# Kernel tuning notes

Hardware: AMD Instinct MI355X
Metric: run time of the kernel (lower is better)

The kernel has to match this reference:

```python
import jax, jax.numpy as jnp
import numpy as np

IN_DIM = 32000   # source vocab
OUT_DIM = 32000  # target vocab
HID = 1024
MAXLEN = 32      # decode steps
B = 64
SRC_LEN = 256


def _lstm_bias(h):
    # Keras LSTM: unit_forget_bias=True -> forget-gate bias = 1, rest 0. Gate order i,f,g,o.
    return jnp.concatenate([jnp.zeros(h), jnp.ones(h), jnp.zeros(2 * h)])


def setup_inputs() -> dict:
    key = jax.random.key(0)
    ks = jax.random.split(key, 12)
    g = lambda k, shape, s=0.02: (jax.random.normal(k, shape, jnp.float32) * s)
    return {
        "source": jax.random.randint(ks[0], (B, SRC_LEN), 0, IN_DIM, jnp.int32),
        "enc_emb": g(ks[1], (IN_DIM, HID)),
        "enc_K": g(ks[2], (HID, 4 * HID)),
        "enc_R": g(ks[3], (HID, 4 * HID)),
        "enc_b": _lstm_bias(HID),
        "dec_emb": g(ks[4], (OUT_DIM, HID)),
        "dec_K": g(ks[5], (HID, 4 * HID)),
        "dec_R": g(ks[6], (HID, 4 * HID)),
        "dec_b": _lstm_bias(HID),
        "W_a": g(ks[7], (HID, HID)),
        "W_c": g(ks[8], (2 * HID, HID)),
        "b_c": jnp.zeros(HID, jnp.float32),
        "W_out": g(ks[9], (HID, OUT_DIM)),
        "b_out": jnp.zeros(OUT_DIM, jnp.float32),
    }


def _lstm_cell(x, h, c, K, R, b):
    z = x @ K + h @ R + b
    i, f, g, o = jnp.split(z, 4, axis=-1)
    c = jax.nn.sigmoid(f) * c + jax.nn.sigmoid(i) * jnp.tanh(g)
    h = jax.nn.sigmoid(o) * jnp.tanh(c)
    return h, c


def reference(source, enc_emb, enc_K, enc_R, enc_b,
              dec_emb, dec_K, dec_R, dec_b,
              W_a, W_c, b_c, W_out, b_out):
    bsz = source.shape[0]
    hid = enc_K.shape[0]

    # ----- Encoder (mask_zero=True: skip state update where source==0) -----
    xe = enc_emb[source]                      # [B,T,H]
    mask = source > 0                         # [B,T]

    def enc_step(carry, xm):
        h, c = carry
        x, m = xm                             # x [B,H], m [B]
        hn, cn = _lstm_cell(x, h, c, enc_K, enc_R, enc_b)
        m = m[:, None]
        return (jnp.where(m, hn, h), jnp.where(m, cn, c)), jnp.where(m, hn, h)

    h0 = jnp.zeros((bsz, hid), xe.dtype)
    (he, ce), hs_t = jax.lax.scan(enc_step, (h0, h0),
                                  (xe.transpose(1, 0, 2), mask.T))
    hs = hs_t.transpose(1, 0, 2)              # [B,T,H] encoder states

    # ----- Decoder loop (greedy argmax feedback) -----
    hsW = hs @ W_a                            # [B,T,H], precomputed attention keys
    amask = mask[:, None, :].astype(hs.dtype)  # [B,1,T]

    def dec_step(carry, _):
        y, h, c = carry                       # y [B] int32
        x = dec_emb[y]                        # [B,H]
        hn, cn = _lstm_cell(x, h, c, dec_K, dec_R, dec_b)
        ht = hn[:, None, :]                   # [B,1,H]
        # Luong attention with source mask (exp -> mask -> normalize, as in source)
        sc = jnp.einsum('bqh,bkh->bqk', ht, hsW)        # [B,1,T]
        sc = jnp.exp(sc - sc.max(-1, keepdims=True)) * amask
        a = sc / sc.sum(-1, keepdims=True)
        ctx = jnp.einsum('bqk,bkh->bqh', a, hs)          # [B,1,H]
        ah = jnp.tanh(jnp.concatenate([ctx, ht], -1) @ W_c + b_c)
        prob = jax.nn.softmax(ah @ W_out + b_out, axis=-1)[:, 0, :]  # [B,V]
        yn = jnp.argmax(prob, axis=-1).astype(jnp.int32)
        return (yn, hn, cn), prob

    y0 = jnp.ones((bsz,), jnp.int32)          # start token = 1 (tf.ones)
    _, outs = jax.lax.scan(dec_step, (y0, he, ce), None, length=MAXLEN)
    return outs.transpose(1, 0, 2)            # [B, MAXLEN, OUT_DIM]
```

## Files before the change

### kernel.cpp

```cpp
#include <hip/hip_runtime.h>
#include <hip/hip_bf16.h>

typedef __hip_bfloat16 bf16;
typedef short bf8v __attribute__((ext_vector_type(8)));
typedef float f32x4 __attribute__((ext_vector_type(4)));

#define DEVINL __device__ __forceinline__
#define MFMA16(a, b, c) __builtin_amdgcn_mfma_f32_16x16x32_bf16((a), (b), (c), 0, 0, 0)

DEVINL float us2f(unsigned short u) { unsigned v = ((unsigned)u) << 16; return __uint_as_float(v); }
DEVINL float b2f(bf16 x) { return __bfloat162float(x); }
DEVINL bf16 f2b(float x) { return __float2bfloat16(x); }
DEVINL float sigf(float x) { return 1.0f / (1.0f + expf(-x)); }
DEVINL unsigned short f2bu(float f) { bf16 h = __float2bfloat16(f); return *(unsigned short*)&h; }

DEVINL void gload16(const void* g, void* l) {
  __builtin_amdgcn_global_load_lds((const __attribute__((address_space(1))) void*)g,
                                   (__attribute__((address_space(3))) void*)l, 16, 0, 0);
}

DEVINL unsigned ald(const unsigned* p) {
  return __hip_atomic_load(p, __ATOMIC_RELAXED, __HIP_MEMORY_SCOPE_AGENT);
}
DEVINL void ast(unsigned* p, unsigned v) {
// ... 9 lines not shown
    unsigned g = blockIdx.x >> 5;
    unsigned* grp = bars + (g * 2 + s) * 16;
    unsigned* top = bars + (16 + s) * 16;
    unsigned* gen = bars + 288;
    unsigned t = __hip_atomic_fetch_add(grp, 1u, __ATOMIC_RELAXED, __HIP_MEMORY_SCOPE_AGENT);
    if (t == 31u) {
      ast(grp, 0u);
      unsigned tt = __hip_atomic_fetch_add(top, 1u, __ATOMIC_RELAXED, __HIP_MEMORY_SCOPE_AGENT);
      if (tt == 7u) {
        ast(top, 0u);
        asm volatile("s_waitcnt vmcnt(0)");
        ast(gen, lgen + 1u);
      }
    }
    while (ald(gen) <= lgen) __builtin_amdgcn_s_sleep(4);
  }
  __syncthreads();
}

#define OKPT_H  ((size_t)0)
#define OKPT_L  ((size_t)8388608)
#define ORPT_H  ((size_t)16777216)
#define ORPT_L  ((size_t)25165824)
#define OWAT    ((size_t)33554432)
#define OXE_H   ((size_t)35651584)
#define OXE_L   ((size_t)69206016)
#define OHSF5   ((size_t)35651584)
#define OHSB5   ((size_t)102760448)
#define XCH     ((size_t)136314880)
#define OHPK_E0 (XCH + 0)
// ... 8 lines not shown
#define OBARS5  (XCH + 1901568)
#define OXK_L5  ((size_t)138412032)
#define OWCT_H  ((size_t)0)
#define OWCT_L  ((size_t)4194304)
#define OPCTX5  ((size_t)8388608)
#define OWOT5   ((size_t)138412032)
#define OKRTH5  ((size_t)203948032)
#define OKRTL5  ((size_t)220725248)
#define OHSW5   ((size_t)237502464)

#define DELTA   1e-4f

#define D_LH   0
#define D_LL   32768
#define D_ZS   65536
#define D_AST  0
#define D_E    0
#define D_HBF  0
#define D_PSC  4096
#define D_EK   8448
#define D_PC4  8704
#define D_ZS3  0
#define D_PSC2 33024
#define D_GMX  37376
#define D_CCN  41536
#define D_CAND 41600
#define D_YL   131072
#define D_INV  131136
#define D_RT   131200

__global__ void ed_zero_v5(float4* p, int n) {
  int i = blockIdx.x * 256 + threadIdx.x;
  if (i < n) p[i] = make_float4(0.f, 0.f, 0.f, 0.f);
}

__global__ void ed_transpose_v5(const float* __restrict__ in, bf16* __restrict__ out,
                                int R, int C, int ostride, int ooff, int perm) {
  __shared__ float tile[32][33];
  int c0 = blockIdx.x * 32, r0 = blockIdx.y * 32;
  int tx = threadIdx.x & 31, ty0 = threadIdx.x >> 5;
#pragma unroll
  for (int i = 0; i < 4; i++) {
    int ty = ty0 + i * 8;
    tile[ty][tx] = in[(size_t)(r0 + ty) * C + c0 + tx];
  }
  __syncthreads();
#pragma unroll
  for (int i = 0; i < 4; i++) {
    int ty = ty0 + i * 8;
    int c = c0 + ty;
    int oc = perm ? ((c & 1023) * 4 + (c >> 10)) : c;
    out[(size_t)oc * ostride + ooff + r0 + tx] = f2b(tile[tx][ty]);
  }
}

__global__ void ed_transpose_split_v5(const float* __restrict__ in, bf16* __restrict__ oh,
                                      bf16* __restrict__ ol, int R, int C, int ostride,
                                      int ooff, int perm) {
  __shared__ float tile[32][33];
  int c0 = blockIdx.x * 32, r0 = blockIdx.y * 32;
  int tx = threadIdx.x & 31, ty0 = threadIdx.x >> 5;
#pragma unroll
  for (int i = 0; i < 4; i++) {
    int ty = ty0 + i * 8;
    tile[ty][tx] = in[(size_t)(r0 + ty) * C + c0 + tx];
  }
  __syncthreads();
#pragma unroll
  for (int i = 0; i < 4; i++) {
    int ty = ty0 + i * 8;
    int c = c0 + ty;
    int oc = perm ? ((c & 1023) * 4 + (c >> 10)) : c;
    float v = tile[tx][ty];
    bf16 hh = f2b(v);
    size_t o = (size_t)oc * ostride + ooff + r0 + tx;
    oh[o] = hh;
    ol[o] = f2b(v - b2f(hh));
  }
}

__global__ void ed_gather_split_v5(const int* __restrict__ src, const float* __restrict__ emb,
                                   bf16* __restrict__ xh, bf16* __restrict__ xl) {
  int bid = blockIdx.x;
  int t = bid >> 6, b = bid & 63;
  int tok = src[b * 256 + t];
  const float* rowp = emb + (size_t)tok * 1024;
  int i = threadIdx.x * 4;
  float4 v = *(const float4*)(rowp + i);
  bf16 h0 = f2b(v.x), h1 = f2b(v.y), h2 = f2b(v.z), h3 = f2b(v.w);
  ushort4 oh, ol;
  oh.x = *(unsigned short*)&h0; oh.y = *(unsigned short*)&h1;
  oh.z = *(unsigned short*)&h2; oh.w = *(unsigned short*)&h3;
  ol.x = f2bu(v.x - b2f(h0)); ol.y = f2bu(v.y - b2f(h1));
  ol.z = f2bu(v.z - b2f(h2)); ol.w = f2bu(v.w - b2f(h3));
  *(ushort4*)(xh + (size_t)bid * 1024 + i) = oh;
  *(ushort4*)(xl + (size_t)bid * 1024 + i) = ol;
}

__global__ __launch_bounds__(256, 2) void ed_gemm_bt_v5(
    const bf16* __restrict__ A, const bf16* __restrict__ BT, bf16* __restrict__ C,
    int M, int N, int K) {
  __shared__ __align__(16) bf16 As[128 * 32];
  __shared__ __align__(16) bf16 Bs[128 * 32];
  int m0 = blockIdx.y * 128, n0 = blockIdx.x * 128;
  int tid = threadIdx.x, w = tid >> 6, l = tid & 63;
  int wm = w >> 1, wn = w & 1;
  int lr = l & 15, lq = l >> 4;
  f32x4 acc[4][4] = {};
  for (int k0 = 0; k0 < K; k0 += 32) {
    __syncthreads();
#pragma unroll
    for (int j = 0; j < 2; j++) {
      int o = (w * 2 + j) * 1024 + l * 16;
      int rrow = o >> 6, kk = (o & 63) >> 1;
// ... 9 lines not shown
        bf8v b = *(const bf8v*)(Bs + (wn * 64 + ni * 16 + lr) * 32 + lq * 8);
        acc[mi][ni] = MFMA16(a, b, acc[mi][ni]);
      }
    }
  }
#pragma unroll
  for (int mi = 0; mi < 4; mi++)
#pragma unroll
    for (int ni = 0; ni < 4; ni++)
#pragma unroll
      for (int r = 0; r < 4; r++)
        C[(size_t)(m0 + wm * 64 + mi * 16 + lq * 4 + r) * N + n0 + wn * 64 + ni * 16 + lr] =
            f2b(acc[mi][ni][r]);
}

__global__ __launch_bounds__(256, 2) void ed_gemm3_v5(
    const bf16* __restrict__ Ah, const bf16* __restrict__ Al,
    const bf16* __restrict__ Bh, const bf16* __restrict__ Bl,
    bf16* __restrict__ Ch, bf16* __restrict__ Cl, int M, int N, int K) {
  __shared__ __align__(16) bf16 Ash[128 * 32];
  __shared__ __align__(16) bf16 Asl[128 * 32];
  __shared__ __align__(16) bf16 Bsh[128 * 32];
  __shared__ __align__(16) bf16 Bsl[128 * 32];
  int m0 = blockIdx.y * 128, n0 = blockIdx.x * 128;
  int tid = threadIdx.x, w = tid >> 6, l = tid & 63;
  int wm = w >> 1, wn = w & 1;
  int lr = l & 15, lq = l >> 4;
  f32x4 acc[4][4] = {};
  for (int k0 = 0; k0 < K; k0 += 32) {
    __syncthreads();
#pragma unroll
// ... 22 lines not shown
  }
#pragma unroll
  for (int mi = 0; mi < 4; mi++)
#pragma unroll
    for (int ni = 0; ni < 4; ni++)
#pragma unroll
      for (int r = 0; r < 4; r++) {
        float v = acc[mi][ni][r];
        bf16 hh = f2b(v);
        size_t idx = (size_t)(m0 + wm * 64 + mi * 16 + lq * 4 + r) * N + n0 + wn * 64 + ni * 16 + lr;
        Ch[idx] = hh;
        Cl[idx] = f2b(v - b2f(hh));
      }
}

__global__ __launch_bounds__(1024, 4) void ed_enc_v5(
    const int* __restrict__ src, const bf16* __restrict__ Rh, const bf16* __restrict__ Rl,
    const bf16* __restrict__ Xh, const bf16* __restrict__ Xl, const float* __restrict__ enc_b,
    unsigned* hpk0, unsigned* hpk1, float* __restrict__ cbuf,
    float* __restrict__ hsf, bf16* __restrict__ hsb, unsigned* bars) {
  extern __shared__ char sm[];
  bf16* lh = (bf16*)sm;
  bf16* ll = (bf16*)(sm + 32768);
  float* zs = (float*)(sm + 65536);
  float* xkf = (float*)(sm + 82944);
  int bid = blockIdx.x, tid = threadIdx.x;
  int bg = bid >> 6, cg = bid & 63;
  int wv = tid >> 6, l = tid & 63, lr = l & 15, lq = l >> 4;
  int kq = wv >> 2, cs = wv & 3;
  int srow = tid >> 6, sj0 = (tid & 63) * 16;
  int grow = tid >> 4, gul = tid & 15;
  bf8v Rh_[8], Rl_[8];
  {
    const bf16* bh = Rh + (size_t)(cg * 64 + cs * 16 + lr) * 1024 + kq * 256 + lq * 8;
    const bf16* bl = Rl + (size_t)(cg * 64 + cs * 16 + lr) * 1024 + kq * 256 + lq * 8;
#pragma unroll
    for (int i = 0; i < 8; i++) {
      Rh_[i] = *(const bf8v*)(bh + i * 32);
      Rl_[i] = *(const bf8v*)(bl + i * 32);
    }
  }
  float bi[4];
// ... 12 lines not shown
      const unsigned* hrow = hc + (size_t)(bg * 16 + srow) * 1024 + sj0;
      unsigned u[16];
#pragma unroll
      for (int j = 0; j < 16; j++) u[j] = ald(hrow + j);
      int r8 = (srow & 7) << 3;
#pragma unroll
      for (int j = 0; j < 16; j += 2) {
        int es = (sj0 + j) ^ r8;
        *(unsigned*)((char*)lh + srow * 2048 + es * 2) = (u[j] >> 16) | (u[j + 1] & 0xffff0000u);
        *(unsigned*)((char*)ll + srow * 2048 + es * 2) = (u[j] & 0xffffu) | (u[j + 1] << 16);
      }
    }
    {
      int xr = tid >> 6, xc = tid & 63;
      size_t xi = ((size_t)t * 64 + bg * 16 + xr) * 4096 + cg * 64 + xc;
      xkf[xr * 64 + xc] = us2f(*(const unsigned short*)(Xh + xi)) +
                          us2f(*(const unsigned short*)(Xl + xi));
    }
    __syncthreads();
    {
      f32x4 acc = {0.f, 0.f, 0.f, 0.f};
      int r8 = (lr & 7) << 3;
#pragma unroll
      for (int i = 0; i < 8; i++) {
        int e0 = kq * 256 + i * 32 + lq * 8;
        int es = e0 ^ r8;
        bf8v a_h = *(const bf8v*)((char*)lh + lr * 2048 + es * 2);
        bf8v a_l = *(const bf8v*)((char*)ll + lr * 2048 + es * 2);
        acc = MFMA16(a_h, Rh_[i], acc);
        acc = MFMA16(a_h, Rl_[i], acc);
        acc = MFMA16(a_l, Rh_[i], acc);
        acc = MFMA16(a_l, Rl_[i], acc);
// ... 12 lines not shown
                zs[(32 + grow) * 68 + cc] + zs[(48 + grow) * 68 + cc] +
                xkf[grow * 64 + cc] + bi[g];
      }
      float iv = sigf(zz[0]), fv = sigf(zz[1]), gv = tanhf(zz[2]), ov = sigf(zz[3]);
      float cn = fv * c_ + iv * gv;
      float hnv = ov * tanhf(cn);
      bool m = src[b_ * 256 + t] > 0;
      int es = u ^ ((grow & 7) << 3);
      float hold = b2f(*(const bf16*)((char*)lh + grow * 2048 + es * 2)) +
                   b2f(*(const bf16*)((char*)ll + grow * 2048 + es * 2));
      float hv = m ? hnv : hold;
      c_ = m ? cn : c_;
      unsigned short uh = f2bu(hv);
      unsigned pkv = ((unsigned)uh << 16) | (unsigned)f2bu(hv - us2f(uh));
      ast(hn + (size_t)b_ * 1024 + u, pkv);
      hsf[((size_t)t * 64 + b_) * 1024 + u] = hv;
      hsb[((size_t)t * 64 + b_) * 1024 + u] = f2b(hv);
    }
    gridbar2(bars, lgen);
    lgen++;
    unsigned* tp = hc; hc = hn; hn = tp;
  }
  if (tid < 256) cbuf[(size_t)(bg * 16 + grow) * 1024 + cg * 16 + gul] = c_;
}

DEVINL void dec_lstm5(int bg, int cgl, int tid, char* sm,
                      const unsigned* hc, unsigned* hn,
                      const float* __restrict__ dec_emb,
                      const bf16* __restrict__ Kh, const bf16* __restrict__ Kl,
                      const float* __restrict__ dec_b, float& c_) {
  {
    int srow = tid >> 6, sj0 = (tid & 63) * 16;
    const unsigned* hrow = hc + (size_t)(bg * 16 + srow) * 1024 + sj0;
    unsigned u[16];
#pragma unroll
    for (int j = 0; j < 16; j++) u[j] = ald(hrow + j);
    int r8 = (srow & 7) << 3;
    bf16* lh = (bf16*)(sm + D_LH);
    bf16* ll = (bf16*)(sm + D_LL);
#pragma unroll
    for (int j = 0; j < 16; j += 2) {
      int es = (sj0 + j) ^ r8;
      *(unsigned*)((char*)lh + srow * 2048 + es * 2) = (u[j] >> 16) | (u[j + 1] & 0xffff0000u);
      *(unsigned*)((char*)ll + srow * 2048 + es * 2) = (u[j] & 0xffffu) | (u[j + 1] << 16);
    }
  }
  __syncthreads();
  int wv = tid >> 6, l = tid & 63, lr = l & 15, lq = l >> 4;
  int kq = wv >> 2, cs = wv & 3;
  const int* y_l = (const int*)(sm + D_YL);
  float* zs = (float*)(sm + D_ZS);
  {
    f32x4 acc = {0.f, 0.f, 0.f, 0.f};
    const bf16* bh = Kh + (size_t)(cgl * 64 + cs * 16 + lr) * 2048;
    const bf16* bl = Kl + (size_t)(cgl * 64 + cs * 16 + lr) * 2048;
    if (kq < 2) {
      const float* xr = dec_emb + (size_t)y_l[lr] * 1024 + kq * 512 + lq * 8;
#pragma unroll 4
      for (int i = 0; i < 16; i++) {
        float4 v0 = *(const float4*)(xr + i * 32);
        float4 v1 = *(const float4*)(xr + i * 32 + 4);
        float vs[8] = {v0.x, v0.y, v0.z, v0.w, v1.x, v1.y, v1.z, v1.w};
        bf8v a_h, a_l;
#pragma unroll
        for (int e = 0; e < 8; e++) {
          unsigned short uh = f2bu(vs[e]);
          a_h[e] = (short)uh;
          a_l[e] = (short)f2bu(vs[e] - us2f(uh));
        }
        int k = kq * 512 + i * 32 + lq * 8;
        bf8v b_h = *(const bf8v*)(bh + k);
        bf8v b_l = *(const bf8v*)(bl + k);
        acc = MFMA16(a_h, b_h, acc); acc = MFMA16(a_h, b_l, acc);
        acc = MFMA16(a_l, b_h, acc); acc = MFMA16(a_l, b_l, acc);
      }
    } else {
      bf16* lh = (bf16*)(sm + D_LH);
      bf16* ll = (bf16*)(sm + D_LL);
      int r8 = (lr & 7) << 3;
#pragma unroll 4
      for (int i = 0; i < 16; i++) {
        int k2 = (kq - 2) * 512 + i * 32 + lq * 8;
        int es = k2 ^ r8;
        bf8v a_h = *(const bf8v*)((char*)lh + lr * 2048 + es * 2);
        bf8v a_l = *(const bf8v*)((char*)ll + lr * 2048 + es * 2);
        int k = 1024 + k2;
        bf8v b_h = *(const bf8v*)(bh + k);
        bf8v b_l = *(const bf8v*)(bl + k);
        acc = MFMA16(a_h, b_h, acc); acc = MFMA16(a_h, b_l, acc);
        acc = MFMA16(a_l, b_h, acc); acc = MFMA16(a_l, b_l, acc);
      }
    }
#pragma unroll
    for (int r = 0; r < 4; r++) zs[(kq * 16 + lq * 4 + r) * 68 + cs * 16 + lr] = acc[r];
  }
  __syncthreads();
  if (tid < 256) {
    int grow = tid >> 4, gul = tid & 15;
    int b_ = bg * 16 + grow;
    float zz[4];
#pragma unroll
    for (int g = 0; g < 4; g++) {
      int cc = gul * 4 + g;
      int colp = cgl * 64 + cc;
      float v = zs[(0 + grow) * 68 + cc] + zs[(16 + grow) * 68 + cc] +
                zs[(32 + grow) * 68 + cc] + zs[(48 + grow) * 68 + cc];
      zz[g] = v + dec_b[(colp & 3) * 1024 + (colp >> 2)];
    }
    float iv = sigf(zz[0]), fv = sigf(zz[1]), gv = tanhf(zz[2]), ov = sigf(zz[3]);
    float cn = fv * c_ + iv * gv;
    c_ = cn;
    float hv = ov * tanhf(cn);
    unsigned short uh = f2bu(hv);
    unsigned pkv = ((unsigned)uh << 16) | (unsigned)f2bu(hv - us2f(uh));
    ast(hn + (size_t)b_ * 1024 + cgl * 16 + gul, pkv);
  }
}

__global__ __launch_bounds__(1024, 4) void ed_dec_v5(
    const int* __restrict__ src,
    const bf16* __restrict__ KRh, const bf16* __restrict__ KRl, const float* __restrict__ dec_b,
    const bf16* __restrict__ WcTh, const bf16* __restrict__ WcTl, const float* __restrict__ b_cp,
    const bf16* __restrict__ WoTh, const float* __restrict__ b_op,
    const float* __restrict__ Wout_f32, const float* __restrict__ dec_emb,
    const float* __restrict__ hsf, const bf16* __restrict__ hsW,
    unsigned* hpkA, unsigned* hpkB, float* __restrict__ cbuf,
    float* __restrict__ pctx, float* __restrict__ psum, unsigned* ahpk,
    float* __restrict__ rowsum, float* __restrict__ rmax, int* __restrict__ ridx,
    float* __restrict__ out, unsigned* bars) {
  extern __shared__ char sm[];
  int bid = blockIdx.x, tid = threadIdx.x;
  int bg = bid >> 6, cgl = bid & 63;
  int wv = tid >> 6, l = tid & 63, lr = l & 15, lq = l >> 4;
  float c_ = 0.f;
  if (tid < 256) c_ = cbuf[(size_t)(bg * 16 + (tid >> 4)) * 1024 + cgl * 16 + (tid & 15)];
  unsigned *hc = hpkA, *hn = hpkB;
  unsigned lgen = 0;

  if (tid < 16) ((int*)(sm + D_YL))[tid] = 1;
  __syncthreads();
  dec_lstm5(bg, cgl, tid, sm, hc, hn, dec_emb, KRh, KRl, dec_b, c_);
  gridbar2(bars, lgen); lgen++;
  { unsigned* tp = hc; hc = hn; hn = tp; }

  for (int st = 0; st < 32; st++) {
    {
      int b_ = bid >> 2, kg = bid & 3;
      float* hbf = (float*)(sm + D_HBF);
      hbf[tid] = us2f((unsigned short)(ald(hc + (size_t)b_ * 1024 + tid) >> 16));
      __syncthreads();
      float* psc = (float*)(sm + D_PSC);
      {
        int kl = tid >> 4, q = tid & 15;
        const bf16* wrow = hsW + ((size_t)(kg * 64 + kl) * 64 + b_) * 1024 + q * 64;
        float p = 0.f;
#pragma unroll
        for (int j = 0; j < 8; j++) {
// ... 31 lines not shown
        pc4[kc * 1024 + cq * 4 + 2] = a2;
        pc4[kc * 1024 + cq * 4 + 3] = a3;
      }
      __syncthreads();
      {
        float v = pc4[tid] + pc4[1024 + tid] + pc4[2048 + tid] + pc4[3072 + tid];
        astf(pctx + ((size_t)kg * 64 + b_) * 1024 + tid, v);
      }
      if (tid == 0) {
        float* ek2 = (float*)(sm + D_EK);
        float s_ = 0.f;
        for (int i2 = 0; i2 < 64; i2++) s_ += ek2[i2];
        astf(psum + kg * 64 + b_, s_);
      }
    }
    gridbar2(bars, lgen); lgen++;
    {
      float* inv_l = (float*)(sm + D_INV);
      if (tid < 16) {
        int rb = bg * 16 + tid;
        float sg = aldf(psum + rb) + aldf(psum + 64 + rb) +
                   aldf(psum + 128 + rb) + aldf(psum + 192 + rb);
        inv_l[tid] = 1.0f / sg;
      }
      __syncthreads();
      float* zs3 = (float*)(sm + D_ZS3);
      {
        int kq = wv;
        f32x4 acc = {0.f, 0.f, 0.f, 0.f};
        const bf16* bh = WcTh + (size_t)(cgl * 16 + lr) * 2048;
        const bf16* bl = WcTl + (size_t)(cgl * 16 + lr) * 2048;
// ... 30 lines not shown
        for (int r = 0; r < 4; r++) zs3[(kq * 16 + lq * 4 + r) * 17 + lr] = acc[r];
      }
      __syncthreads();
      if (tid < 256) {
        int grow = tid >> 4, gcol = tid & 15;
        float v = 0.f;
#pragma unroll
        for (int q = 0; q < 16; q++) v += zs3[(q * 16 + grow) * 17 + gcol];
        v += b_cp[cgl * 16 + gcol];
        float ahv = tanhf(v);
        unsigned short uh = f2bu(ahv);
        unsigned pkv = ((unsigned)uh << 16) | (unsigned)f2bu(ahv - us2f(uh));
        ast(ahpk + (size_t)(bg * 16 + grow) * 1024 + cgl * 16 + gcol, pkv);
      }
    }
    gridbar2(bars, lgen); lgen++;
    {
      int base = bid * 125;
      bf16* Ast = (bf16*)(sm + D_AST);
      {
        int row = tid >> 4, k0 = (tid & 15) * 64;
        const unsigned* ap = ahpk + (size_t)row * 1024 + k0;
        int r8 = (row & 7) << 3;
#pragma unroll
        for (int j = 0; j < 64; j += 2) {
          unsigned u0 = ald(ap + j), u1 = ald(ap + j + 1);
          int es = (k0 + j) ^ r8;
          *(unsigned*)((char*)Ast + row * 2048 + es * 2) = (u0 >> 16) | (u1 & 0xffff0000u);
        }
      }
      __syncthreads();
      int rg = wv >> 2, cg2 = wv & 3;
      f32x4 la0 = {0.f, 0.f, 0.f, 0.f}, la1 = {0.f, 0.f, 0.f, 0.f};
      {
        int c0 = cg2 * 32 + lr;      int cc0 = c0 < 125 ? c0 : 124;
        int c1 = cg2 * 32 + 16 + lr; int cc1 = c1 < 125 ? c1 : 124;
        const bf16* w0 = WoTh + (size_t)(base + cc0) * 1024;
        const bf16* w1 = WoTh + (size_t)(base + cc1) * 1024;
        int r8 = ((rg * 16 + lr) & 7) << 3;
#pragma unroll 4
        for (int i = 0; i < 32; i++) {
          int k = i * 32 + lq * 8;
          int es = k ^ r8;
          bf8v a_h = *(const bf8v*)((char*)Ast + (rg * 16 + lr) * 2048 + es * 2);
          la0 = MFMA16(a_h, *(const bf8v*)(w0 + k), la0);
          la1 = MFMA16(a_h, *(const bf8v*)(w1 + k), la1);
        }
      }
      __syncthreads();
      float* e = (float*)(sm + D_E);
      {
#pragma unroll
        for (int ct = 0; ct < 2; ct++) {
          int cl = cg2 * 32 + ct * 16 + lr;
          if (cl < 125) {
#pragma unroll
            for (int r = 0; r < 4; r++) {
              float lv = (ct == 0 ? la0[r] : la1[r]) + b_op[base + cl];
              e[(rg * 16 + lq * 4 + r) * 129 + cl] = lv;
            }
          }
        }
      }
      __syncthreads();
      if (tid < 64) {
        float sm_ = 0.f, v1 = -1e30f, v2 = -1e30f;
        int i1 = 0, i2 = 0;
        for (int c2 = 0; c2 < 125; c2++) {
          float v = e[tid * 129 + c2];
          sm_ += expf(v);
          if (v > v1) { v2 = v1; i2 = i1; v1 = v; i1 = base + c2; }
          else if (v > v2) { v2 = v; i2 = base + c2; }
        }
        astf(rowsum + bid * 64 + tid, sm_);
        astf(rmax + (bid * 64 + tid) * 2 + 0, v1);
        ast((unsigned*)ridx + (bid * 64 + tid) * 2 + 0, (unsigned)i1);
        astf(rmax + (bid * 64 + tid) * 2 + 1, v2);
        ast((unsigned*)ridx + (bid * 64 + tid) * 2 + 1, (unsigned)i2);
      }
    }
    gridbar2(bars, lgen); lgen++;
    {
      float* psc2 = (float*)(sm + D_PSC2);
      {
        int rr = tid & 63, pp = tid >> 6;
        float s_ = 0.f;
#pragma unroll 4
        for (int cu = pp * 16; cu < pp * 16 + 16; cu++) s_ += aldf(rowsum + cu * 64 + rr);
        psc2[rr * 17 + pp] = s_;
      }
      __syncthreads();
      float* rt = (float*)(sm + D_RT);
      if (tid < 64) {
        float s_ = 0.f;
#pragma unroll
        for (int p2 = 0; p2 < 16; p2++) s_ += psc2[tid * 17 + p2];
        rt[tid] = s_;
      }
      __syncthreads();
      float* e = (float*)(sm + D_E);
      {
        int base = bid * 125;
        for (int i = tid; i < 8000; i += 1024) {
          int r_ = i / 125, c2 = i - r_ * 125;
          out[((size_t)r_ * 32 + st) * 32000 + base + c2] = expf(e[r_ * 129 + c2]) / rt[r_];
        }
      }
      if (st < 31) {
        float* gmx = (float*)(sm + D_GMX);
        int* ccnt = (int*)(sm + D_CCN);
        int* cand = (int*)(sm + D_CAND);
        int* y_l = (int*)(sm + D_YL);
        int r16 = tid & 15, ch = tid >> 4;
        int rowg = bg * 16 + r16;
        float vloc[8]; int iloc[8];
        {
          float m_ = -1e30f;
#pragma unroll
          for (int ee = 0; ee < 8; ee++) {
            int ent = ch * 8 + ee;
// ... 22 lines not shown
            }
          }
        }
        __syncthreads();
        {
          int row2 = wv;
          int rowg2 = bg * 16 + row2;
          int cnt = ccnt[row2]; if (cnt > 8) cnt = 8;
          double bv = -1e30; int bi_ = 0x7fffffff;
          for (int ci = 0; ci < cnt; ci++) {
            int c = cand[row2 * 8 + ci];
            double s_ = 0.0;
            for (int k = l; k < 1024; k += 64) {
              unsigned u = ald(ahpk + (size_t)rowg2 * 1024 + k);
              float av = us2f((unsigned short)(u >> 16)) + us2f((unsigned short)(u & 0xffffu));
              s_ += (double)av * (double)Wout_f32[(size_t)k * 32000 + c];
            }
#pragma unroll
            for (int off = 32; off > 0; off >>= 1) s_ += __shfl_down(s_, off);
            if (l == 0) {
              s_ += (double)b_op[c];
              if (s_ > bv || (s_ == bv && c < bi_)) { bv = s_; bi_ = c; }
            }
          }
          if (l == 0) y_l[row2] = bi_;
        }
        __syncthreads();
        dec_lstm5(bg, cgl, tid, sm, hc, hn, dec_emb, KRh, KRl, dec_b, c_);
      }
    }
    gridbar2(bars, lgen); lgen++;
    { unsigned* tp = hc; hc = hn; hn = tp; }
  }
}

extern "C" void kernel_launch(void* const* d_in, const int* in_sizes, int n_in,
                              void* d_out, int out_size, void* d_ws, size_t ws_size,
                              hipStream_t stream) {
  (void)in_sizes; (void)n_in; (void)out_size; (void)ws_size;
  const int*   src     = (const int*)  d_in[0];
  const float* enc_emb = (const float*)d_in[1];
  const float* enc_K   = (const float*)d_in[2];
  const float* enc_R   = (const float*)d_in[3];
  const float* enc_b   = (const float*)d_in[4];
  const float* dec_emb = (const float*)d_in[5];
  const float* dec_K   = (const float*)d_in[6];
  const float* dec_R   = (const float*)d_in[7];
  const float* dec_b   = (const float*)d_in[8];
  const float* W_a     = (const float*)d_in[9];
  const float* W_c     = (const float*)d_in[10];
  const float* b_c     = (const float*)d_in[11];
  const float* W_out   = (const float*)d_in[12];
  const float* b_out   = (const float*)d_in[13];
  char* ws = (char*)d_ws;

  hipFuncSetAttribute((const void*)ed_enc_v5, hipFuncAttributeMaxDynamicSharedMemorySize, 163840);
  hipFuncSetAttribute((const void*)ed_dec_v5, hipFuncAttributeMaxDynamicSharedMemorySize, 163840);

  bf16* KpTh = (bf16*)(ws + OKPT_H);
  bf16* KpTl = (bf16*)(ws + OKPT_L);
  bf16* RpTh = (bf16*)(ws + ORPT_H);
  bf16* RpTl = (bf16*)(ws + ORPT_L);
  bf16* WaT  = (bf16*)(ws + OWAT);
  bf16* xeh  = (bf16*)(ws + OXE_H);
  bf16* xel  = (bf16*)(ws + OXE_L);
  float* hsf = (float*)(ws + OHSF5);
  bf16* hsb  = (bf16*)(ws + OHSB5);
  unsigned* hpkE0 = (unsigned*)(ws + OHPK_E0);
  unsigned* hpkE1 = (unsigned*)(ws + OHPK_E1);
  unsigned* hpkD0 = (unsigned*)(ws + OHPK_D0);
  float* cbuf = (float*)(ws + OCBUF5);
  unsigned* ahpk = (unsigned*)(ws + OAHPK);
  float* rsum = (float*)(ws + ORSUM5);
  float* rmaxp = (float*)(ws + ORMAX5);
  int*  ridxp = (int*)(ws + ORIDX5);
  float* psum = (float*)(ws + OPSUM5);
  unsigned* bars = (unsigned*)(ws + OBARS5);
  bf16* XkL  = (bf16*)(ws + OXK_L5);
  bf16* XkH  = (bf16*)d_out;
  bf16* WcTh = (bf16*)(ws + OWCT_H);
  bf16* WcTl = (bf16*)(ws + OWCT_L);
  float* pctx = (float*)(ws + OPCTX5);
  bf16* WoTh = (bf16*)(ws + OWOT5);
  bf16* KRTh = (bf16*)(ws + OKRTH5);
  bf16* KRTl = (bf16*)(ws + OKRTL5);
  bf16* hsW  = (bf16*)(ws + OHSW5);

  ed_zero_v5<<<512, 256, 0, stream>>>((float4*)(ws + XCH), 131072);
  ed_transpose_split_v5<<<dim3(128, 32), 256, 0, stream>>>(enc_K, KpTh, KpTl, 1024, 4096, 1024, 0, 1);
  ed_transpose_split_v5<<<dim3(128, 32), 256, 0, stream>>>(enc_R, RpTh, RpTl, 1024, 4096, 1024, 0, 1);
  ed_transpose_v5<<<dim3(32, 32), 256, 0, stream>>>(W_a, WaT, 1024, 1024, 1024, 0, 0);
  ed_gather_split_v5<<<16384, 256, 0, stream>>>(src, enc_emb, xeh, xel);
  ed_gemm3_v5<<<dim3(32, 128), 256, 0, stream>>>(xeh, xel, KpTh, KpTl, XkH, XkL, 16384, 4096, 1024);
  ed_transpose_split_v5<<<dim3(32, 64), 256, 0, stream>>>(W_c, WcTh, WcTl, 2048, 1024, 2048, 0, 0);
  ed_enc_v5<<<256, 1024, 87040, stream>>>(src, RpTh, RpTl, XkH, XkL, enc_b,
                                          hpkE0, hpkE1, cbuf, hsf, hsb, bars);
  ed_transpose_v5<<<dim3(1000, 32), 256, 0, stream>>>(W_out, WoTh, 1024, 32000, 1024, 0, 0);
  ed_transpose_split_v5<<<dim3(128, 32), 256, 0, stream>>>(dec_K, KRTh, KRTl, 1024, 4096, 2048, 0, 1);
  ed_transpose_split_v5<<<dim3(128, 32), 256, 0, stream>>>(dec_R, KRTh, KRTl, 1024, 4096, 2048, 1024, 1);
  ed_gemm_bt_v5<<<dim3(8, 128), 256, 0, stream>>>(hsb, WaT, hsW, 16384, 1024, 1024);
  ed_dec_v5<<<256, 1024, 131456, stream>>>(src, KRTh, KRTl, dec_b, WcTh, WcTl, b_c,
                                           WoTh, b_out, W_out, dec_emb, hsf, hsW,
                                           hpkE0, hpkD0, cbuf, pctx, psum, ahpk,
                                           rsum, rmaxp, ridxp, (float*)d_out, bars + 512);
}
```

Measured before the change: 15.11 ms.

## Use per-batch-group 64-block barriers and stage LSTM/logit weights through LDS

```diff
diff --git a/kernel.cpp b/kernel.cpp
--- a/kernel.cpp
+++ b/kernel.cpp
@@ -47,6 +47,28 @@
       }
     }
     while (ald(gen) <= lgen) __builtin_amdgcn_s_sleep(4);
+  }
+  __syncthreads();
+}
+
+DEVINL void bar64(unsigned* b, unsigned lgen, int lid) {
+  __syncthreads();
+  if (threadIdx.x == 0) {
+    unsigned s = lgen & 1;
+    unsigned* grp = b + (((unsigned)(lid >> 5) & 1u) * 2 + s) * 16;
+    unsigned* top = b + (4 + s) * 16;
+    unsigned* gen = b + 96;
+    unsigned t = __hip_atomic_fetch_add(grp, 1u, __ATOMIC_RELAXED, __HIP_MEMORY_SCOPE_AGENT);
+    if (t == 31u) {
+      ast(grp, 0u);
+      unsigned tt = __hip_atomic_fetch_add(top, 1u, __ATOMIC_RELAXED, __HIP_MEMORY_SCOPE_AGENT);
+      if (tt == 1u) {
+        ast(top, 0u);
+        asm volatile("s_waitcnt vmcnt(0)");
+        ast(gen, lgen + 1u);
+      }
+    }
+    while (ald(gen) <= lgen) __builtin_amdgcn_s_sleep(2);
   }
   __syncthreads();
 }
@@ -85,27 +107,30 @@
 #define D_LH   0
 #define D_LL   32768
 #define D_ZS   65536
-#define D_AST  0
-#define D_E    0
+#define D_KBH  83968
+#define D_KBL  116736
+#define D4_A   0
+#define D4_W   16384
+#define D4_E   49152
 #define D_HBF  0
 #define D_PSC  4096
 #define D_EK   8448
 #define D_PC4  8704
 #define D_ZS3  0
-#define D_PSC2 33024
-#define D_GMX  37376
-#define D_CCN  41536
-#define D_CAND 41600
-#define D_YL   131072
-#define D_INV  131136
-#define D_RT   131200
-
-__global__ void ed_zero_v5(float4* p, int n) {
+#define D_PSC2 0
+#define D_GMX  4352
+#define D_CCN  8512
+#define D_CAND 8576
+#define D_YL   149504
+#define D_INV  149568
+#define D_RT   149632
+
+__global__ void ed_zero_v6(float4* p, int n) {
   int i = blockIdx.x * 256 + threadIdx.x;
   if (i < n) p[i] = make_float4(0.f, 0.f, 0.f, 0.f);
 }
 
-__global__ void ed_transpose_v5(const float* __restrict__ in, bf16* __restrict__ out,
+__global__ void ed_transpose_v6(const float* __restrict__ in, bf16* __restrict__ out,
                                 int R, int C, int ostride, int ooff, int perm) {
   __shared__ float tile[32][33];
   int c0 = blockIdx.x * 32, r0 = blockIdx.y * 32;
@@ -125,7 +150,7 @@
   }
 }
 
-__global__ void ed_transpose_split_v5(const float* __restrict__ in, bf16* __restrict__ oh,
+__global__ void ed_transpose_split_v6(const float* __restrict__ in, bf16* __restrict__ oh,
                                       bf16* __restrict__ ol, int R, int C, int ostride,
                                       int ooff, int perm) {
   __shared__ float tile[32][33];
@@ -150,7 +175,7 @@
   }
 }
 
-__global__ void ed_gather_split_v5(const int* __restrict__ src, const float* __restrict__ emb,
+__global__ void ed_gather_split_v6(const int* __restrict__ src, const float* __restrict__ emb,
                                    bf16* __restrict__ xh, bf16* __restrict__ xl) {
   int bid = blockIdx.x;
   int t = bid >> 6, b = bid & 63;
@@ -168,7 +193,7 @@
   *(ushort4*)(xl + (size_t)bid * 1024 + i) = ol;
 }
 
-__global__ __launch_bounds__(256, 2) void ed_gemm_bt_v5(
+__global__ __launch_bounds__(256, 2) void ed_gemm_bt_v6(
     const bf16* __restrict__ A, const bf16* __restrict__ BT, bf16* __restrict__ C,
     int M, int N, int K) {
   __shared__ __align__(16) bf16 As[128 * 32];
@@ -208,7 +233,7 @@
             f2b(acc[mi][ni][r]);
 }
 
-__global__ __launch_bounds__(256, 2) void ed_gemm3_v5(
+__global__ __launch_bounds__(256, 2) void ed_gemm3_v6(
     const bf16* __restrict__ Ah, const bf16* __restrict__ Al,
     const bf16* __restrict__ Bh, const bf16* __restrict__ Bl,
     bf16* __restrict__ Ch, bf16* __restrict__ Cl, int M, int N, int K) {
@@ -261,18 +286,19 @@
       }
 }
 
-__global__ __launch_bounds__(1024, 4) void ed_enc_v5(
+__global__ __launch_bounds__(1024, 4) void ed_enc_v6(
     const int* __restrict__ src, const bf16* __restrict__ Rh, const bf16* __restrict__ Rl,
     const bf16* __restrict__ Xh, const bf16* __restrict__ Xl, const float* __restrict__ enc_b,
     unsigned* hpk0, unsigned* hpk1, float* __restrict__ cbuf,
-    float* __restrict__ hsf, bf16* __restrict__ hsb, unsigned* bars) {
+    float* __restrict__ hsf, bf16* __restrict__ hsb, unsigned* barsE) {
   extern __shared__ char sm[];
   bf16* lh = (bf16*)sm;
   bf16* ll = (bf16*)(sm + 32768);
   float* zs = (float*)(sm + 65536);
   float* xkf = (float*)(sm + 82944);
   int bid = blockIdx.x, tid = threadIdx.x;
-  int bg = bid >> 6, cg = bid & 63;
+  int bg = bid >> 6, cg = bid & 63, lid = bid & 63;
+  unsigned* barL = barsE + bg * 128;
   int wv = tid >> 6, l = tid & 63, lr = l & 15, lq = l >> 4;
   int kq = wv >> 2, cs = wv & 3;
   int srow = tid >> 6, sj0 = (tid & 63) * 16;
@@ -315,8 +341,9 @@
     {
       int xr = tid >> 6, xc = tid & 63;
       size_t xi = ((size_t)t * 64 + bg * 16 + xr) * 4096 + cg * 64 + xc;
-      xkf[xr * 64 + xc] = us2f(*(const unsigned short*)(Xh + xi)) +
-                          us2f(*(const unsigned short*)(Xl + xi));
+      unsigned short xh = __builtin_nontemporal_load((const unsigned short*)(Xh + xi));
+      unsigned short xl = __builtin_nontemporal_load((const unsigned short*)(Xl + xi));
+      xkf[xr * 64 + xc] = us2f(xh) + us2f(xl);
     }
     __syncthreads();
     {
@@ -359,86 +386,98 @@
       unsigned short uh = f2bu(hv);
       unsigned pkv = ((unsigned)uh << 16) | (unsigned)f2bu(hv - us2f(uh));
       ast(hn + (size_t)b_ * 1024 + u, pkv);
-      hsf[((size_t)t * 64 + b_) * 1024 + u] = hv;
-      hsb[((size_t)t * 64 + b_) * 1024 + u] = f2b(hv);
-    }
-    gridbar2(bars, lgen);
+      __builtin_nontemporal_store(hv, hsf + ((size_t)t * 64 + b_) * 1024 + u);
+      __builtin_nontemporal_store(f2bu(hv), (unsigned short*)(hsb + ((size_t)t * 64 + b_) * 1024 + u));
+    }
+    bar64(barL, lgen, lid);
     lgen++;
     unsigned* tp = hc; hc = hn; hn = tp;
   }
   if (tid < 256) cbuf[(size_t)(bg * 16 + grow) * 1024 + cg * 16 + gul] = c_;
 }
 
-DEVINL void dec_lstm5(int bg, int cgl, int tid, char* sm,
+DEVINL void dec_lstm6(int bg, int cgl, int tid, char* sm,
                       const unsigned* hc, unsigned* hn,
                       const float* __restrict__ dec_emb,
                       const bf16* __restrict__ Kh, const bf16* __restrict__ Kl,
                       const float* __restrict__ dec_b, float& c_) {
+  bf16* lh = (bf16*)(sm + D_LH);
+  bf16* ll = (bf16*)(sm + D_LL);
   {
-    int srow = tid >> 6, sj0 = (tid & 63) * 16;
-    const unsigned* hrow = hc + (size_t)(bg * 16 + srow) * 1024 + sj0;
+    int srow = tid >> 6, sl = tid & 63;
+    const unsigned* hrow = hc + (size_t)(bg * 16 + srow) * 1024 + sl * 16;
     unsigned u[16];
 #pragma unroll
     for (int j = 0; j < 16; j++) u[j] = ald(hrow + j);
-    int r8 = (srow & 7) << 3;
-    bf16* lh = (bf16*)(sm + D_LH);
-    bf16* ll = (bf16*)(sm + D_LL);
-#pragma unroll
-    for (int j = 0; j < 16; j += 2) {
-      int es = (sj0 + j) ^ r8;
-      *(unsigned*)((char*)lh + srow * 2048 + es * 2) = (u[j] >> 16) | (u[j + 1] & 0xffff0000u);
-      *(unsigned*)((char*)ll + srow * 2048 + es * 2) = (u[j] & 0xffffu) | (u[j + 1] << 16);
-    }
-  }
-  __syncthreads();
+    uint4 ha, hb, la, lb;
+    ha.x = (u[0] >> 16) | (u[1] & 0xffff0000u);  ha.y = (u[2] >> 16) | (u[3] & 0xffff0000u);
+    ha.z = (u[4] >> 16) | (u[5] & 0xffff0000u);  ha.w = (u[6] >> 16) | (u[7] & 0xffff0000u);
+    hb.x = (u[8] >> 16) | (u[9] & 0xffff0000u);  hb.y = (u[10] >> 16) | (u[11] & 0xffff0000u);
+    hb.z = (u[12] >> 16) | (u[13] & 0xffff0000u); hb.w = (u[14] >> 16) | (u[15] & 0xffff0000u);
+    la.x = (u[0] & 0xffffu) | (u[1] << 16);  la.y = (u[2] & 0xffffu) | (u[3] << 16);
+    la.z = (u[4] & 0xffffu) | (u[5] << 16);  la.w = (u[6] & 0xffffu) | (u[7] << 16);
+    lb.x = (u[8] & 0xffffu) | (u[9] << 16);  lb.y = (u[10] & 0xffffu) | (u[11] << 16);
+    lb.z = (u[12] & 0xffffu) | (u[13] << 16); lb.w = (u[14] & 0xffffu) | (u[15] << 16);
+    int swz = (srow & 7) << 4;
+    char* rbh = (char*)lh + srow * 2048;
+    char* rbl = (char*)ll + srow * 2048;
+    *(uint4*)(rbh + ((sl * 32) ^ swz)) = ha;
+    *(uint4*)(rbh + ((sl * 32 + 16) ^ swz)) = hb;
+    *(uint4*)(rbl + ((sl * 32) ^ swz)) = la;
+    *(uint4*)(rbl + ((sl * 32 + 16) ^ swz)) = lb;
+  }
   int wv = tid >> 6, l = tid & 63, lr = l & 15, lq = l >> 4;
-  int kq = wv >> 2, cs = wv & 3;
+  int kg2 = wv >> 2, cs = wv & 3;
+  bf16* kbh = (bf16*)(sm + D_KBH);
+  bf16* kbl = (bf16*)(sm + D_KBL);
   const int* y_l = (const int*)(sm + D_YL);
   float* zs = (float*)(sm + D_ZS);
-  {
-    f32x4 acc = {0.f, 0.f, 0.f, 0.f};
-    const bf16* bh = Kh + (size_t)(cgl * 64 + cs * 16 + lr) * 2048;
-    const bf16* bl = Kl + (size_t)(cgl * 64 + cs * 16 + lr) * 2048;
-    if (kq < 2) {
-      const float* xr = dec_emb + (size_t)y_l[lr] * 1024 + kq * 512 + lq * 8;
-#pragma unroll 4
-      for (int i = 0; i < 16; i++) {
-        float4 v0 = *(const float4*)(xr + i * 32);
-        float4 v1 = *(const float4*)(xr + i * 32 + 4);
+  f32x4 acc = {0.f, 0.f, 0.f, 0.f};
+  int colB = cs * 16 + lr;
+  int bswz = (colB & 7) << 4;
+  int aswz = (lr & 7) << 4;
+  for (int c = 0; c < 8; c++) {
+    __syncthreads();
+#pragma unroll
+    for (int r = 0; r < 2; r++) {
+      int i = wv * 128 + r * 64 + l;
+      int col = i >> 5, j = i & 31;
+      size_t se = (size_t)(cgl * 64 + col) * 2048 + c * 256 + ((size_t)(j ^ (col & 7)) << 3);
+      gload16(Kh + se, (char*)kbh + wv * 2048 + r * 1024);
+      gload16(Kl + se, (char*)kbl + wv * 2048 + r * 1024);
+    }
+    __syncthreads();
+#pragma unroll
+    for (int s = 0; s < 2; s++) {
+      int kl = kg2 * 64 + s * 32 + lq * 8;
+      bf8v b_h = *(const bf8v*)((char*)kbh + colB * 512 + ((kl * 2) ^ bswz));
+      bf8v b_l = *(const bf8v*)((char*)kbl + colB * 512 + ((kl * 2) ^ bswz));
+      int gk = c * 256 + kl;
+      bf8v a_h, a_l;
+      if (gk < 1024) {
+        const float* xr = dec_emb + (size_t)y_l[lr] * 1024 + gk;
+        float4 v0 = *(const float4*)xr;
+        float4 v1 = *(const float4*)(xr + 4);
         float vs[8] = {v0.x, v0.y, v0.z, v0.w, v1.x, v1.y, v1.z, v1.w};
-        bf8v a_h, a_l;
 #pragma unroll
         for (int e = 0; e < 8; e++) {
           unsigned short uh = f2bu(vs[e]);
           a_h[e] = (short)uh;
           a_l[e] = (short)f2bu(vs[e] - us2f(uh));
         }
-        int k = kq * 512 + i * 32 + lq * 8;
-        bf8v b_h = *(const bf8v*)(bh + k);
-        bf8v b_l = *(const bf8v*)(bl + k);
-        acc = MFMA16(a_h, b_h, acc); acc = MFMA16(a_h, b_l, acc);
-        acc = MFMA16(a_l, b_h, acc); acc = MFMA16(a_l, b_l, acc);
-      }
-    } else {
-      bf16* lh = (bf16*)(sm + D_LH);
-      bf16* ll = (bf16*)(sm + D_LL);
-      int r8 = (lr & 7) << 3;
-#pragma unroll 4
-      for (int i = 0; i < 16; i++) {
-        int k2 = (kq - 2) * 512 + i * 32 + lq * 8;
-        int es = k2 ^ r8;
-        bf8v a_h = *(const bf8v*)((char*)lh + lr * 2048 + es * 2);
-        bf8v a_l = *(const bf8v*)((char*)ll + lr * 2048 + es * 2);
-        int k = 1024 + k2;
-        bf8v b_h = *(const bf8v*)(bh + k);
-        bf8v b_l = *(const bf8v*)(bl + k);
-        acc = MFMA16(a_h, b_h, acc); acc = MFMA16(a_h, b_l, acc);
-        acc = MFMA16(a_l, b_h, acc); acc = MFMA16(a_l, b_l, acc);
-      }
-    }
-#pragma unroll
-    for (int r = 0; r < 4; r++) zs[(kq * 16 + lq * 4 + r) * 68 + cs * 16 + lr] = acc[r];
-  }
+      } else {
+        int hk = gk - 1024;
+        a_h = *(const bf8v*)((char*)lh + lr * 2048 + ((hk * 2) ^ aswz));
+        a_l = *(const bf8v*)((char*)ll + lr * 2048 + ((hk * 2) ^ aswz));
+      }
+      acc = MFMA16(a_h, b_h, acc);
+      acc = MFMA16(a_h, b_l, acc);
+      acc = MFMA16(a_l, b_h, acc);
+      acc = MFMA16(a_l, b_l, acc);
+    }
+  }
+#pragma unroll
+  for (int r = 0; r < 4; r++) zs[(kg2 * 16 + lq * 4 + r) * 68 + cs * 16 + lr] = acc[r];
   __syncthreads();
   if (tid < 256) {
     int grow = tid >> 4, gul = tid & 15;
@@ -462,7 +501,7 @@
   }
 }
 
-__global__ __launch_bounds__(1024, 4) void ed_dec_v5(
+__global__ __launch_bounds__(1024, 4) void ed_dec_v6(
     const int* __restrict__ src,
     const bf16* __restrict__ KRh, const bf16* __restrict__ KRl, const float* __restrict__ dec_b,
     const bf16* __restrict__ WcTh, const bf16* __restrict__ WcTl, const float* __restrict__ b_cp,
@@ -472,20 +511,21 @@
     unsigned* hpkA, unsigned* hpkB, float* __restrict__ cbuf,
     float* __restrict__ pctx, float* __restrict__ psum, unsigned* ahpk,
     float* __restrict__ rowsum, float* __restrict__ rmax, int* __restrict__ ridx,
-    float* __restrict__ out, unsigned* bars) {
+    float* __restrict__ out, unsigned* barsG, unsigned* barsL) {
   extern __shared__ char sm[];
   int bid = blockIdx.x, tid = threadIdx.x;
-  int bg = bid >> 6, cgl = bid & 63;
+  int bg = bid >> 6, cgl = bid & 63, lid = bid & 63;
+  unsigned* barL = barsL + bg * 128;
   int wv = tid >> 6, l = tid & 63, lr = l & 15, lq = l >> 4;
   float c_ = 0.f;
   if (tid < 256) c_ = cbuf[(size_t)(bg * 16 + (tid >> 4)) * 1024 + cgl * 16 + (tid & 15)];
   unsigned *hc = hpkA, *hn = hpkB;
-  unsigned lgen = 0;
+  unsigned lgenL = 0, lgenG = 0;
 
   if (tid < 16) ((int*)(sm + D_YL))[tid] = 1;
   __syncthreads();
-  dec_lstm5(bg, cgl, tid, sm, hc, hn, dec_emb, KRh, KRl, dec_b, c_);
-  gridbar2(bars, lgen); lgen++;
+  dec_lstm6(bg, cgl, tid, sm, hc, hn, dec_emb, KRh, KRl, dec_b, c_);
+  bar64(barL, lgenL, lid); lgenL++;
   { unsigned* tp = hc; hc = hn; hn = tp; }
 
   for (int st = 0; st < 32; st++) {
@@ -547,7 +587,7 @@
         astf(psum + kg * 64 + b_, s_);
       }
     }
-    gridbar2(bars, lgen); lgen++;
+    bar64(barL, lgenL, lid); lgenL++;
     {
       float* inv_l = (float*)(sm + D_INV);
       if (tid < 16) {
@@ -608,52 +648,63 @@
         ast(ahpk + (size_t)(bg * 16 + grow) * 1024 + cgl * 16 + gcol, pkv);
       }
     }
-    gridbar2(bars, lgen); lgen++;
+    gridbar2(barsG, lgenG); lgenG++;
     {
       int base = bid * 125;
-      bf16* Ast = (bf16*)(sm + D_AST);
+      bf16* abuf = (bf16*)(sm + D4_A);
+      bf16* wbuf = (bf16*)(sm + D4_W);
+      int rg = wv >> 2, cpair = wv & 3;
+      f32x4 acc0 = {0.f, 0.f, 0.f, 0.f}, acc1 = {0.f, 0.f, 0.f, 0.f};
+      for (int kc = 0; kc < 8; kc++) {
+        int k0 = kc * 128;
+        __syncthreads();
+        {
+          int row = tid >> 4, l16 = tid & 15;
+          const unsigned* ap = ahpk + (size_t)row * 1024 + k0 + l16 * 8;
+          unsigned u0 = ald(ap), u1 = ald(ap + 1), u2 = ald(ap + 2), u3 = ald(ap + 3);
+          unsigned u4 = ald(ap + 4), u5 = ald(ap + 5), u6 = ald(ap + 6), u7 = ald(ap + 7);
+          uint4 hv;
+          hv.x = (u0 >> 16) | (u1 & 0xffff0000u);
+          hv.y = (u2 >> 16) | (u3 & 0xffff0000u);
+          hv.z = (u4 >> 16) | (u5 & 0xffff0000u);
+          hv.w = (u6 >> 16) | (u7 & 0xffff0000u);
+          *(uint4*)((char*)abuf + row * 256 + ((l16 * 16) ^ ((row & 7) << 4))) = hv;
+        }
+#pragma unroll
+        for (int r = 0; r < 2; r++) {
+          int i = wv * 128 + r * 64 + l;
+          int col = i >> 4, j = i & 15;
+          int ccol = col < 125 ? col : 124;
+          size_t se = (size_t)(base + ccol) * 1024 + k0 + ((size_t)(j ^ (col & 7)) << 3);
+          gload16(WoTh + se, (char*)wbuf + wv * 2048 + r * 1024);
+        }
+        __syncthreads();
+#pragma unroll
+        for (int s = 0; s < 4; s++) {
+          int kl = s * 32 + lq * 8;
+          int ar = rg * 16 + lr;
+          bf8v a = *(const bf8v*)((char*)abuf + ar * 256 + ((kl * 2) ^ ((ar & 7) << 4)));
+          int c0 = cpair * 32 + lr, c1 = c0 + 16;
+          bf8v b0 = *(const bf8v*)((char*)wbuf + c0 * 256 + ((kl * 2) ^ ((c0 & 7) << 4)));
+          bf8v b1 = *(const bf8v*)((char*)wbuf + c1 * 256 + ((kl * 2) ^ ((c1 & 7) << 4)));
+          acc0 = MFMA16(a, b0, acc0);
+          acc1 = MFMA16(a, b1, acc1);
+        }
+      }
+      __syncthreads();
+      float* e = (float*)(sm + D4_E);
       {
-        int row = tid >> 4, k0 = (tid & 15) * 64;
-        const unsigned* ap = ahpk + (size_t)row * 1024 + k0;
-        int r8 = (row & 7) << 3;
-#pragma unroll
-        for (int j = 0; j < 64; j += 2) {
-          unsigned u0 = ald(ap + j), u1 = ald(ap + j + 1);
-          int es = (k0 + j) ^ r8;
-          *(unsigned*)((char*)Ast + row * 2048 + es * 2) = (u0 >> 16) | (u1 & 0xffff0000u);
-        }
-      }
-      __syncthreads();
-      int rg = wv >> 2, cg2 = wv & 3;
-      f32x4 la0 = {0.f, 0.f, 0.f, 0.f}, la1 = {0.f, 0.f, 0.f, 0.f};
-      {
-        int c0 = cg2 * 32 + lr;      int cc0 = c0 < 125 ? c0 : 124;
-        int c1 = cg2 * 32 + 16 + lr; int cc1 = c1 < 125 ? c1 : 124;
-        const bf16* w0 = WoTh + (size_t)(base + cc0) * 1024;
-        const bf16* w1 = WoTh + (size_t)(base + cc1) * 1024;
-        int r8 = ((rg * 16 + lr) & 7) << 3;
-#pragma unroll 4
-        for (int i = 0; i < 32; i++) {
-          int k = i * 32 + lq * 8;
-          int es = k ^ r8;
-          bf8v a_h = *(const bf8v*)((char*)Ast + (rg * 16 + lr) * 2048 + es * 2);
-          la0 = MFMA16(a_h, *(const bf8v*)(w0 + k), la0);
-          la1 = MFMA16(a_h, *(const bf8v*)(w1 + k), la1);
-        }
-      }
-      __syncthreads();
-      float* e = (float*)(sm + D_E);
-      {
-#pragma unroll
-        for (int ct = 0; ct < 2; ct++) {
-          int cl = cg2 * 32 + ct * 16 + lr;
-          if (cl < 125) {
-#pragma unroll
-            for (int r = 0; r < 4; r++) {
-              float lv = (ct == 0 ? la0[r] : la1[r]) + b_op[base + cl];
-              e[(rg * 16 + lq * 4 + r) * 129 + cl] = lv;
-            }
-          }
+        int cl0 = cpair * 32 + lr;
+        if (cl0 < 125) {
+#pragma unroll
+          for (int r = 0; r < 4; r++)
+            e[(rg * 16 + lq * 4 + r) * 129 + cl0] = acc0[r] + b_op[base + cl0];
+        }
+        int cl1 = cpair * 32 + 16 + lr;
+        if (cl1 < 125) {
+#pragma unroll
+          for (int r = 0; r < 4; r++)
+            e[(rg * 16 + lq * 4 + r) * 129 + cl1] = acc1[r] + b_op[base + cl1];
         }
       }
       __syncthreads();
@@ -673,7 +724,7 @@
         ast((unsigned*)ridx + (bid * 64 + tid) * 2 + 1, (unsigned)i2);
       }
     }
-    gridbar2(bars, lgen); lgen++;
+    gridbar2(barsG, lgenG); lgenG++;
     {
       float* psc2 = (float*)(sm + D_PSC2);
       {
@@ -692,12 +743,13 @@
         rt[tid] = s_;
       }
       __syncthreads();
-      float* e = (float*)(sm + D_E);
+      float* e = (float*)(sm + D4_E);
       {
         int base = bid * 125;
         for (int i = tid; i < 8000; i += 1024) {
           int r_ = i / 125, c2 = i - r_ * 125;
-          out[((size_t)r_ * 32 + st) * 32000 + base + c2] = expf(e[r_ * 129 + c2]) / rt[r_];
+          float pv = expf(e[r_ * 129 + c2]) / rt[r_];
+          __builtin_nontemporal_store(pv, out + ((size_t)r_ * 32 + st) * 32000 + base + c2);
         }
       }
       if (st < 31) {
@@ -750,7 +802,8 @@
             for (int k = l; k < 1024; k += 64) {
               unsigned u = ald(ahpk + (size_t)rowg2 * 1024 + k);
               float av = us2f((unsigned short)(u >> 16)) + us2f((unsigned short)(u & 0xffffu));
-              s_ += (double)av * (double)Wout_f32[(size_t)k * 32000 + c];
+              float wv_ = __builtin_nontemporal_load(Wout_f32 + (size_t)k * 32000 + c);
+              s_ += (double)av * (double)wv_;
             }
 #pragma unroll
             for (int off = 32; off > 0; off >>= 1) s_ += __shfl_down(s_, off);
@@ -762,10 +815,10 @@
           if (l == 0) y_l[row2] = bi_;
         }
         __syncthreads();
-        dec_lstm5(bg, cgl, tid, sm, hc, hn, dec_emb, KRh, KRl, dec_b, c_);
-      }
-    }
-    gridbar2(bars, lgen); lgen++;
+        dec_lstm6(bg, cgl, tid, sm, hc, hn, dec_emb, KRh, KRl, dec_b, c_);
+      }
+    }
+    bar64(barL, lgenL, lid); lgenL++;
     { unsigned* tp = hc; hc = hn; hn = tp; }
   }
 }
@@ -790,8 +843,8 @@
   const float* b_out   = (const float*)d_in[13];
   char* ws = (char*)d_ws;
 
-  hipFuncSetAttribute((const void*)ed_enc_v5, hipFuncAttributeMaxDynamicSharedMemorySize, 163840);
-  hipFuncSetAttribute((const void*)ed_dec_v5, hipFuncAttributeMaxDynamicSharedMemorySize, 163840);
+  hipFuncSetAttribute((const void*)ed_enc_v6, hipFuncAttributeMaxDynamicSharedMemorySize, 163840);
+  hipFuncSetAttribute((const void*)ed_dec_v6, hipFuncAttributeMaxDynamicSharedMemorySize, 163840);
 
   bf16* KpTh = (bf16*)(ws + OKPT_H);
   bf16* KpTl = (bf16*)(ws + OKPT_L);
@@ -811,7 +864,9 @@
   float* rmaxp = (float*)(ws + ORMAX5);
   int*  ridxp = (int*)(ws + ORIDX5);
   float* psum = (float*)(ws + OPSUM5);
-  unsigned* bars = (unsigned*)(ws + OBARS5);
+  unsigned* barsE = (unsigned*)(ws + OBARS5);
+  unsigned* barsG = (unsigned*)(ws + OBARS5 + 4096);
+  unsigned* barsL = (unsigned*)(ws + OBARS5 + 8192);
   bf16* XkL  = (bf16*)(ws + OXK_L5);
   bf16* XkH  = (bf16*)d_out;
   bf16* WcTh = (bf16*)(ws + OWCT_H);
@@ -822,21 +877,21 @@
   bf16* KRTl = (bf16*)(ws + OKRTL5);
   bf16* hsW  = (bf16*)(ws + OHSW5);
 
-  ed_zero_v5<<<512, 256, 0, stream>>>((float4*)(ws + XCH), 131072);
-  ed_transpose_split_v5<<<dim3(128, 32), 256, 0, stream>>>(enc_K, KpTh, KpTl, 1024, 4096, 1024, 0, 1);
-  ed_transpose_split_v5<<<dim3(128, 32), 256, 0, stream>>>(enc_R, RpTh, RpTl, 1024, 4096, 1024, 0, 1);
-  ed_transpose_v5<<<dim3(32, 32), 256, 0, stream>>>(W_a, WaT, 1024, 1024, 1024, 0, 0);
-  ed_gather_split_v5<<<16384, 256, 0, stream>>>(src, enc_emb, xeh, xel);
-  ed_gemm3_v5<<<dim3(32, 128), 256, 0, stream>>>(xeh, xel, KpTh, KpTl, XkH, XkL, 16384, 4096, 1024);
-  ed_transpose_split_v5<<<dim3(32, 64), 256, 0, stream>>>(W_c, WcTh, WcTl, 2048, 1024, 2048, 0, 0);
-  ed_enc_v5<<<256, 1024, 87040, stream>>>(src, RpTh, RpTl, XkH, XkL, enc_b,
-                                          hpkE0, hpkE1, cbuf, hsf, hsb, bars);
-  ed_transpose_v5<<<dim3(1000, 32), 256, 0, stream>>>(W_out, WoTh, 1024, 32000, 1024, 0, 0);
-  ed_transpose_split_v5<<<dim3(128, 32), 256, 0, stream>>>(dec_K, KRTh, KRTl, 1024, 4096, 2048, 0, 1);
-  ed_transpose_split_v5<<<dim3(128, 32), 256, 0, stream>>>(dec_R, KRTh, KRTl, 1024, 4096, 2048, 1024, 1);
-  ed_gemm_bt_v5<<<dim3(8, 128), 256, 0, stream>>>(hsb, WaT, hsW, 16384, 1024, 1024);
-  ed_dec_v5<<<256, 1024, 131456, stream>>>(src, KRTh, KRTl, dec_b, WcTh, WcTl, b_c,
+  ed_zero_v6<<<512, 256, 0, stream>>>((float4*)(ws + XCH), 131072);
+  ed_transpose_split_v6<<<dim3(128, 32), 256, 0, stream>>>(enc_K, KpTh, KpTl, 1024, 4096, 1024, 0, 1);
+  ed_transpose_split_v6<<<dim3(128, 32), 256, 0, stream>>>(enc_R, RpTh, RpTl, 1024, 4096, 1024, 0, 1);
+  ed_transpose_v6<<<dim3(32, 32), 256, 0, stream>>>(W_a, WaT, 1024, 1024, 1024, 0, 0);
+  ed_gather_split_v6<<<16384, 256, 0, stream>>>(src, enc_emb, xeh, xel);
+  ed_gemm3_v6<<<dim3(32, 128), 256, 0, stream>>>(xeh, xel, KpTh, KpTl, XkH, XkL, 16384, 4096, 1024);
+  ed_transpose_split_v6<<<dim3(32, 64), 256, 0, stream>>>(W_c, WcTh, WcTl, 2048, 1024, 2048, 0, 0);
+  ed_enc_v6<<<256, 1024, 87040, stream>>>(src, RpTh, RpTl, XkH, XkL, enc_b,
+                                          hpkE0, hpkE1, cbuf, hsf, hsb, barsE);
+  ed_transpose_v6<<<dim3(1000, 32), 256, 0, stream>>>(W_out, WoTh, 1024, 32000, 1024, 0, 0);
+  ed_transpose_split_v6<<<dim3(128, 32), 256, 0, stream>>>(dec_K, KRTh, KRTl, 1024, 4096, 2048, 0, 1);
+  ed_transpose_split_v6<<<dim3(128, 32), 256, 0, stream>>>(dec_R, KRTh, KRTl, 1024, 4096, 2048, 1024, 1);
+  ed_gemm_bt_v6<<<dim3(8, 128), 256, 0, stream>>>(hsb, WaT, hsW, 16384, 1024, 1024);
+  ed_dec_v6<<<256, 1024, 150528, stream>>>(src, KRTh, KRTl, dec_b, WcTh, WcTl, b_c,
                                            WoTh, b_out, W_out, dec_emb, hsf, hsW,
                                            hpkE0, hpkD0, cbuf, pctx, psum, ahpk,
-                                           rsum, rmaxp, ridxp, (float*)d_out, bars + 512);
-}
+                                           rsum, rmaxp, ridxp, (float*)d_out, barsG, barsL);
+}
```

After: 13.90 ms. -8.0%, faster.
